# Kernel optimization log

Hardware: AMD Instinct MI355X
Metric: run time of the kernel (lower is better)

## Reference

```python
import jax, jax.numpy as jnp
import numpy as np

B, T, D, H, O = 256, 512, 256, 1024, 256


def _uniform(key, shape, fan_in):
    # kaiming_uniform with a=0.1: bound = sqrt(6 / ((1 + a^2) * fan_in))
    bound = float(np.sqrt(6.0 / ((1.0 + 0.1 ** 2) * fan_in)))
    return jax.random.uniform(key, shape, jnp.float32, -bound, bound)


def setup_inputs() -> dict:
    key = jax.random.key(0)
    ks = jax.random.split(key, 8)
    inp = {
        "x": jax.random.normal(ks[0], (B, T, D), jnp.float32),
        "W_gx": _uniform(ks[1], (D, H), D),
        "W_gh": _uniform(ks[2], (H, H), H),
        "b_g": jnp.zeros((H,), jnp.float32),
        "W_ix": _uniform(ks[3], (D, H), D),
        "W_ih": _uniform(ks[4], (H, H), H),
        "b_i": jnp.zeros((H,), jnp.float32),
        "W_fx": _uniform(ks[5], (D, H), D),
        "W_fh": _uniform(ks[6], (H, H), H),
        "b_f": jnp.zeros((H,), jnp.float32),
        "W_ox": _uniform(jax.random.fold_in(key, 10), (D, H), D),
        "W_oh": _uniform(jax.random.fold_in(key, 11), (H, H), H),
        "b_o": jnp.zeros((H,), jnp.float32),
        "W_ph": _uniform(ks[7], (H, O), H),
        "b_p": jnp.zeros((O,), jnp.float32),
    }
    return inp


def reference(x, W_gx, W_gh, b_g, W_ix, W_ih, b_i, W_fx, W_fh, b_f,
              W_ox, W_oh, b_o, W_ph, b_p):
    Hd = W_gh.shape[0]
    # Fuse the 4 per-gate matmuls into two GEMMs (same math as the loop).
    Wx = jnp.concatenate([W_gx, W_ix, W_fx, W_ox], axis=1)  # [D, 4H]
    Wh = jnp.concatenate([W_gh, W_ih, W_fh, W_oh], axis=1)  # [H, 4H]
    b = jnp.concatenate([b_g, b_i, b_f, b_o])               # [4H]
    xW = jnp.einsum('btd,dk->tbk', x, Wx) + b                # [T, B, 4H]

    def step(carry, xw_t):
        h, c = carry
        z = xw_t + h @ Wh                                    # [B, 4H]
        g = jnp.tanh(z[:, :Hd])
        i = jax.nn.sigmoid(z[:, Hd:2 * Hd])
        f = jax.nn.sigmoid(z[:, 2 * Hd:3 * Hd])
        o = jax.nn.sigmoid(z[:, 3 * Hd:])
        c = g * i + c * f
        h = jnp.tanh(c) * o
        return (h, c), None

    h0 = jnp.zeros((x.shape[0], Hd), x.dtype)
    (h, _), _ = jax.lax.scan(step, (h0, h0), xW)
    return jax.nn.softmax(h @ W_ph + b_p, axis=1)
```

## Files before the change

### kernel.cpp

```cpp
#include <hip/hip_runtime.h>


typedef _Float16 f16;
typedef _Float16 f16x8 __attribute__((ext_vector_type(8)));
typedef _Float16 f16x4 __attribute__((ext_vector_type(4)));
typedef float f32x4 __attribute__((ext_vector_type(4)));
typedef unsigned int u32;

#define WS_WT    0
#define WS_WPHT  10485760
#define WS_HBUF  11010048
#define WS_LG    12058624
#define WS_CNT   12320768
#define WS_TICK  12322816
#define WS_XH    16777216
#define WS_XH_END 83886080

#define ZB    81920u
#define BCAST 114688

__device__ __forceinline__ float sigm(float v) { return 1.0f / (1.0f + __expf(-v)); }
__device__ __forceinline__ float tanhfast(float v) {
  float t = __expf(-2.0f * fabsf(v));
  float r = (1.0f - t) / (1.0f + t);
  return v < 0.0f ? -r : r;
}

__global__ __launch_bounds__(256) void prep_wt(
    const float* __restrict__ Wgh, const float* __restrict__ Wih,
    const float* __restrict__ Wfh, const float* __restrict__ Woh,
    const float* __restrict__ Wgx, const float* __restrict__ Wix,
    const float* __restrict__ Wfx, const float* __restrict__ Wox,
    f16* __restrict__ WT)
{
  __shared__ float tile[32][33];
  int bid = blockIdx.x;
  int gate = bid / 1280;
  int rem  = bid % 1280;
  int jt = rem / 40, kt = rem % 40;
  const float* srcH = (gate==0)?Wgh:(gate==1)?Wih:(gate==2)?Wfh:Woh;
  const float* srcX = (gate==0)?Wgx:(gate==1)?Wix:(gate==2)?Wfx:Wox;
  const float* src = (kt < 32) ? (srcH + (size_t)(kt*32)*1024)
                               : (srcX + (size_t)(kt*32 - 1024)*1024);
  int t = threadIdx.x;
  {
    int jl = t & 31, kg = t >> 5;
#pragma unroll
    for (int it = 0; it < 4; ++it) {
      int kl = kg + it*8;
      tile[kl][jl] = src[(size_t)kl*1024 + jt*32 + jl];
    }
  }
  __syncthreads();
  {
    int kl = t & 31, jg = t >> 5;
#pragma unroll
    for (int it = 0; it < 4; ++it) {
      int jl2 = jg + it*8;
      WT[(size_t)(gate*1024 + jt*32 + jl2)*1280 + kt*32 + kl] = (f16)tile[kl][jl2];
    }
  }
}

__global__ __launch_bounds__(256) void prep_wph(const float* __restrict__ Wph,
                                                f16* __restrict__ WphT)
{
  __shared__ float tile[32][33];
  int bid = blockIdx.x;
  int jt = bid & 7, kt = bid >> 3;
  int t = threadIdx.x;
  {
    int jl = t & 31, kg = t >> 5;
#pragma unroll
    for (int it = 0; it < 4; ++it) {
      int kl = kg + it*8;
      tile[kl][jl] = Wph[(size_t)(kt*32 + kl)*256 + jt*32 + jl];
    }
  }
  __syncthreads();
  {
    int kl = t & 31, jg = t >> 5;
#pragma unroll
    for (int it = 0; it < 4; ++it) {
      int jl2 = jg + it*8;
      WphT[(size_t)(jt*32 + jl2)*1024 + kt*32 + kl] = (f16)tile[kl][jl2];
    }
  }
}

__global__ __launch_bounds__(256) void prep_x16(const float* __restrict__ x,
                                                f16* __restrict__ xh)
{
  size_t i = ((size_t)blockIdx.x*256 + threadIdx.x) * 16;
  const float4* src = (const float4*)(x + i);
  f16x4* dst = (f16x4*)(xh + i);
#pragma unroll
  for (int j = 0; j < 4; ++j) {
    float4 v = src[j];
    f16x4 h; h[0]=(f16)v.x; h[1]=(f16)v.y; h[2]=(f16)v.z; h[3]=(f16)v.w;
    dst[j] = h;
  }
}

__global__ __launch_bounds__(512, 2) void lstm_main(
    const float* __restrict__ x, const f16* __restrict__ xh, int use_xh,
    const f16* __restrict__ WT, const f16* __restrict__ WphT,
    f16* __restrict__ hbuf,
    const float* __restrict__ bgp, const float* __restrict__ bip,
    const float* __restrict__ bfp, const float* __restrict__ bop,
    const float* __restrict__ bpp, float* __restrict__ lg,
    u32* __restrict__ cnt, u32* __restrict__ tick, float* __restrict__ out)
{
  __shared__ __align__(16) char smem[114704];
  const int tid  = threadIdx.x;
  const int lane = tid & 63;
  const int wv   = tid >> 6;
  const int hgrp = wv & 1;
  const int kh   = wv >> 1;
  const int l15 = lane & 15, l4 = lane >> 4;

  u32 myxcd;
  asm volatile("s_getreg_b32 %0, hwreg(HW_REG_XCC_ID)" : "=s"(myxcd));
  myxcd &= 7u;
  if (tid == 0) {
    u32 t = __hip_atomic_fetch_add(tick + myxcd, 1u,
                                   __ATOMIC_RELAXED, __HIP_MEMORY_SCOPE_AGENT);
    *(volatile u32*)(smem + BCAST) = t;
  }
  if (wv == 0) {
    u32 v = 0;
    int guard = 0;
    for (;;) {
      v = (lane < 8) ? __hip_atomic_load(tick + lane, __ATOMIC_RELAXED,
                                         __HIP_MEMORY_SCOPE_AGENT) : 0u;
      u32 sum = v;
      sum += __shfl_xor(sum, 1);
      sum += __shfl_xor(sum, 2);
      sum += __shfl_xor(sum, 4);
      if (__shfl(sum, 0) == 256u) break;
      __builtin_amdgcn_s_sleep(1);
      if (++guard > (1 << 20)) break;
    }
    int even = __all((lane < 8) ? (v == 32u) : 1);
    if (lane == 0) *(volatile u32*)(smem + BCAST + 4) = (u32)even;
  }
  __syncthreads();
  const bool xloc = (*(volatile u32*)(smem + BCAST + 4)) != 0u;
  const u32 myticket = *(volatile u32*)(smem + BCAST);
  const int xg = xloc ? (int)myxcd    : (blockIdx.x & 7);
  const int cg = xloc ? (int)myticket : (blockIdx.x >> 3);
  u32* flg = cnt + xg*64;

  f16x8 Breg[10][4];
  {
    const int gate = l15 & 3, hsub = l15 >> 2;
#pragma unroll
    for (int f = 0; f < 4; ++f) {
      const int n = gate*1024 + cg*32 + hgrp*16 + f*4 + hsub;
      const f16* wb = WT + (size_t)n*1280 + kh*320 + l4*8;
#pragma unroll
      for (int kk = 0; kk < 10; ++kk) {
        Breg[kk][f] = *(const f16x8*)(wb + kk*32);
        asm volatile("" : "+v"(Breg[kk][f]));
      }
    }
  }

  const int bcol = cg*32 + (tid & 31);
  const float bgr = bgp[bcol], bir = bip[bcol], bfr = bfp[bcol], bor = bop[bcol];

  const u32 aoff = (u32)l15*2560u + (u32)(kh*640 + l4*16);
  const u32 aswz = (u32)l15 << 4;
  const int srow = tid >> 5;
  const int sseg = tid & 31;
  const u32 swzr = (u32)srow << 4;

  float cA = 0.0f, cB = 0.0f;

  u32 pre = 0xFFFFFFFFu;
  bool preOK = false;

#pragma unroll 1
  for (int slot = 0; slot < 1024; ++slot) {
    const int T = slot & 1, s = slot >> 1;
    const u32 Abase = (u32)T * 40960u;
    u32* flgT = flg + T*32;
    const int grow = xg*32 + T*16 + srow;

    if (use_xh) {
      const char* xrow = (const char*)xh + ((size_t)grow*512 + (size_t)s)*512;
      uint4 v = *(const uint4*)(xrow + sseg*16);
      *(uint4*)(smem + Abase + (((u32)srow*2560u + 2048u + (u32)sseg*16u) ^ swzr)) = v;
    } else {
      const float* xsrc = x + ((size_t)grow*512 + (size_t)s)*256;
      float4 xv0 = *(const float4*)(xsrc + (sseg     )*4);
      float4 xv1 = *(const float4*)(xsrc + (sseg + 32)*4);
      f16x4 hv;
      hv[0] = (f16)xv0.x; hv[1] = (f16)xv0.y; hv[2] = (f16)xv0.z; hv[3] = (f16)xv0.w;
      *(f16x4*)(smem + Abase + (((u32)srow*2560u + 2048u + 8u*(u32)(sseg     )) ^ swzr)) = hv;
      hv[0] = (f16)xv1.x; hv[1] = (f16)xv1.y; hv[2] = (f16)xv1.z; hv[3] = (f16)xv1.w;
      *(f16x4*)(smem + Abase + (((u32)srow*2560u + 2048u + 8u*(u32)(sseg + 32)) ^ swzr)) = hv;
    }
    if (s > 0 && !preOK) {
      const u32 tgt = (u32)s;
      u32 v = tgt;
      int guard = 0;
      for (;;) {
        if (lane < 32)
          v = __hip_atomic_load(flgT + lane, __ATOMIC_RELAXED,
                                __HIP_MEMORY_SCOPE_AGENT);
        if (__all(v >= tgt)) break;
        __builtin_amdgcn_s_sleep(1);
        if (++guard > (1 << 18)) break;
      }
      if (lane == 0) {
        if (xloc) { asm volatile("buffer_inv sc0\n\ts_waitcnt vmcnt(0)" ::: "memory"); }
        else      { __threadfence(); }
      }
    }
    {
      const f16* hsrc = hbuf + (size_t)(s & 1)*262144 + (size_t)grow*1024;
#pragma unroll
      for (int j = 0; j < 4; ++j) {
        int chunk = sseg + 32*j;
        uint4 v = *(const uint4*)(hsrc + chunk*8);
        *(uint4*)(smem + Abase + (((u32)srow*2560u + 16u*(u32)chunk) ^ swzr)) = v;
      }
    }
    __syncthreads();
    f32x4 acc0 = {}, acc1 = {}, acc2 = {}, acc3 = {};
#pragma unroll
    for (int kk = 0; kk < 10; ++kk) {
      f16x8 av = *(const f16x8*)(smem + Abase + ((aoff + (u32)kk*64u) ^ aswz));
      acc0 = __builtin_amdgcn_mfma_f32_16x16x32_f16(Breg[kk][0], av, acc0, 0, 0, 0);
      acc1 = __builtin_amdgcn_mfma_f32_16x16x32_f16(Breg[kk][1], av, acc1, 0, 0, 0);
      acc2 = __builtin_amdgcn_mfma_f32_16x16x32_f16(Breg[kk][2], av, acc2, 0, 0, 0);
      acc3 = __builtin_amdgcn_mfma_f32_16x16x32_f16(Breg[kk][3], av, acc3, 0, 0, 0);
    }
    {
      const int nT = (slot + 1) & 1, nS = (slot + 1) >> 1;
      pre = 0xFFFFFFFFu;
      if (nS > 0 && nS < 512 && lane < 32)
        pre = __hip_atomic_load(flg + nT*32 + lane, __ATOMIC_RELAXED,
                                __HIP_MEMORY_SCOPE_AGENT);
    }
    {
      const u32 zkh = ZB + (u32)kh*8192u;
#pragma unroll
      for (int f = 0; f < 4; ++f) {
        const u32 hcol = (u32)(hgrp*16 + f*4 + l4);
        const u32 s16 = ((u32)(l15*32) + hcol) ^ ((u32)(l15 & 7));
        f32x4 acc = (f==0)?acc0:(f==1)?acc1:(f==2)?acc2:acc3;
        *(f32x4*)(smem + zkh + s16*16u) = acc;
      }
    }
    __syncthreads();
    {
      f16* hw = hbuf + (size_t)((s & 1) ^ 1)*262144;
      const int row = tid >> 5, hcol = tid & 31;
      const u32 s16 = ((u32)(row*32) + (u32)hcol) ^ ((u32)(row & 7));
      const u32 ro = s16*16u;
      f32x4 z0 = *(const f32x4*)(smem + ZB +        ro);
      f32x4 z1 = *(const f32x4*)(smem + ZB + 8192u  + ro);
      f32x4 z2 = *(const f32x4*)(smem + ZB + 16384u + ro);
      f32x4 z3 = *(const f32x4*)(smem + ZB + 24576u + ro);
      float zg = z0[0] + z1[0] + z2[0] + z3[0] + bgr;
      float zi = z0[1] + z1[1] + z2[1] + z3[1] + bir;
      float zf = z0[2] + z1[2] + z2[2] + z3[2] + bfr;
      float zo = z0[3] + z1[3] + z2[3] + z3[3] + bor;
      float cv = T ? cB : cA;
      float gv = tanhfast(zg);
      float iv = sigm(zi);
      float fv = sigm(zf);
      float ov = sigm(zo);
      float cn = gv*iv + cv*fv;
      if (T) cB = cn; else cA = cn;
      hw[(size_t)(xg*32 + T*16 + row)*1024 + cg*32 + hcol] = (f16)(tanhfast(cn) * ov);
    }
    {
      const int nS = (slot + 1) >> 1;
      bool ok = (nS >= 512) || __all(pre >= (u32)nS);
      preOK = xloc && ok;
      if (preOK && nS < 512 && lane == 0) {
        asm volatile("buffer_inv sc0\n\ts_waitcnt vmcnt(0)" ::: "memory");
      }
    }
    __syncthreads();
    if (tid == 0) {
      if (!xloc) __threadfence();
      __hip_atomic_store(flgT + cg, (u32)(s + 1),
                         __ATOMIC_RELAXED, __HIP_MEMORY_SCOPE_AGENT);
    }
  }

  if (wv == 0) {
    u32 v = 512u;
    int guard = 0;
    for (;;) {
      v = __hip_atomic_load(flg + lane, __ATOMIC_RELAXED,
                            __HIP_MEMORY_SCOPE_AGENT);
      if (__all(v >= 512u)) break;
      __builtin_amdgcn_s_sleep(1);
      if (++guard > (1 << 18)) break;
    }
    if (lane == 0) {
      if (xloc) { asm volatile("buffer_inv sc0\n\ts_waitcnt vmcnt(0)" ::: "memory"); }
      else      { __threadfence(); }
    }
  }
  __syncthreads();
  {
#pragma unroll 1
    for (int p = 0; p < 32; ++p) {
      int rowl = wv*4 + (p >> 3);
      int oc   = p & 7;
      const f16* hp = hbuf + (size_t)(xg*32 + rowl)*1024 + lane*16;
      const f16* wp = WphT + (size_t)(cg*8 + oc)*1024 + lane*16;
      f16x8 h0 = *(const f16x8*)hp;
      f16x8 h1 = *(const f16x8*)(hp + 8);
      f16x8 w0 = *(const f16x8*)wp;
      f16x8 w1 = *(const f16x8*)(wp + 8);
      float sum = 0.f;
#pragma unroll
      for (int q = 0; q < 8; ++q)
        sum += (float)h0[q]*(float)w0[q] + (float)h1[q]*(float)w1[q];
#pragma unroll
      for (int d = 1; d < 64; d <<= 1) sum += __shfl_xor(sum, d);
      if (lane == 0)
        lg[(size_t)(xg*32 + rowl)*256 + cg*8 + oc] = sum + bpp[cg*8 + oc];
    }
  }
  __syncthreads();
  if (tid == 0) {
    if (!xloc) __threadfence();
    __hip_atomic_store(flg + cg, 513u, __ATOMIC_RELAXED, __HIP_MEMORY_SCOPE_AGENT);
  }
  if (wv == 0) {
    u32 v = 513u;
    int guard = 0;
    for (;;) {
      if (lane < 32)
        v = __hip_atomic_load(flg + lane, __ATOMIC_RELAXED, __HIP_MEMORY_SCOPE_AGENT);
      if (__all(v >= 513u)) break;
      __builtin_amdgcn_s_sleep(1);
      if (++guard > (1 << 18)) break;
    }
    if (lane == 0) {
      if (xloc) { asm volatile("buffer_inv sc0\n\ts_waitcnt vmcnt(0)" ::: "memory"); }
      else      { __threadfence(); }
    }
  }
  __syncthreads();
  if (tid < 64) {
    int rowg = xg*32 + cg;
    const float* lr = lg + (size_t)rowg*256;
    float v0 = lr[tid], v1 = lr[tid+64], v2 = lr[tid+128], v3 = lr[tid+192];
    float mx = fmaxf(fmaxf(v0, v1), fmaxf(v2, v3));
#pragma unroll
    for (int d = 1; d < 64; d <<= 1) mx = fmaxf(mx, __shfl_xor(mx, d));
    float e0 = __expf(v0-mx), e1 = __expf(v1-mx), e2 = __expf(v2-mx), e3 = __expf(v3-mx);
    float sm = e0+e1+e2+e3;
#pragma unroll
    for (int d = 1; d < 64; d <<= 1) sm += __shfl_xor(sm, d);
    float inv = 1.0f / sm;
    float* orow = out + (size_t)rowg*256;
    orow[tid]      = e0*inv;
    orow[tid+64]   = e1*inv;
    orow[tid+128]  = e2*inv;
    orow[tid+192]  = e3*inv;
  }
}

extern "C" void kernel_launch(void* const* d_in, const int* in_sizes, int n_in,
                              void* d_out, int out_size, void* d_ws, size_t ws_size,
                              hipStream_t stream) {
  (void)in_sizes; (void)n_in; (void)out_size;
  const float* x   = (const float*)d_in[0];
  const float* Wgx = (const float*)d_in[1];
  const float* Wgh = (const float*)d_in[2];
  const float* bg  = (const float*)d_in[3];
  const float* Wix = (const float*)d_in[4];
  const float* Wih = (const float*)d_in[5];
  const float* bi  = (const float*)d_in[6];
  const float* Wfx = (const float*)d_in[7];
  const float* Wfh = (const float*)d_in[8];
  const float* bf  = (const float*)d_in[9];
  const float* Wox = (const float*)d_in[10];
  const float* Woh = (const float*)d_in[11];
  const float* bo  = (const float*)d_in[12];
  const float* Wph = (const float*)d_in[13];
  const float* bp  = (const float*)d_in[14];

  char* ws = (char*)d_ws;
  f16*   WT   = (f16*)(ws + WS_WT);
  f16*   WphT = (f16*)(ws + WS_WPHT);
  f16*   hbuf = (f16*)(ws + WS_HBUF);
  float* lg   = (float*)(ws + WS_LG);
  u32*   cnt  = (u32*)(ws + WS_CNT);
  u32*   tick = (u32*)(ws + WS_TICK);
  const int use_xh = (ws_size >= (size_t)WS_XH_END) ? 1 : 0;
  f16*   xh   = (f16*)(ws + WS_XH);

  hipMemsetAsync(hbuf, 0, 524288, stream);
  hipMemsetAsync(cnt, 0, 2048 + 64, stream);

  prep_wt<<<5120, 256, 0, stream>>>(Wgh, Wih, Wfh, Woh, Wgx, Wix, Wfx, Wox, WT);
  prep_wph<<<256, 256, 0, stream>>>(Wph, WphT);
  if (use_xh)
    prep_x16<<<8192, 256, 0, stream>>>(x, xh);
  lstm_main<<<256, 512, 0, stream>>>(x, xh, use_xh, WT, WphT, hbuf,
                                     bg, bi, bf, bo, bp,
                                     lg, cnt, tick, (float*)d_out);
}
```

Measured before the change: 2.468 ms.

## Load MFMA A-operands directly from global into registers, drop LDS staging

Each wave now loads its h and x fragments for the MFMA straight from global memory (hbuf and xh/x) into registers, in the layout the MFMA expects. This replaces staging them through a swizzled LDS tile and removes the __syncthreads before the matmul. LDS shrinks to the reduction and broadcast area. The cost is uncoalesced 16-byte global reads per lane, repeated across the waves that share rows, in exchange for fewer LDS round trips and one fewer block-wide barrier per step.

```diff
diff --git a/kernel.cpp b/kernel.cpp
--- a/kernel.cpp
+++ b/kernel.cpp
@@ -16,8 +16,8 @@
 #define WS_XH    16777216
 #define WS_XH_END 83886080
 
-#define ZB    81920u
-#define BCAST 114688
+#define ZB    0u
+#define BCAST 32768
 
 __device__ __forceinline__ float sigm(float v) { return 1.0f / (1.0f + __expf(-v)); }
 __device__ __forceinline__ float tanhfast(float v) {
@@ -111,7 +111,7 @@
     const float* __restrict__ bpp, float* __restrict__ lg,
     u32* __restrict__ cnt, u32* __restrict__ tick, float* __restrict__ out)
 {
-  __shared__ __align__(16) char smem[114704];
+  __shared__ __align__(16) char smem[32784];
   const int tid  = threadIdx.x;
   const int lane = tid & 63;
   const int wv   = tid >> 6;
@@ -169,12 +169,6 @@
   const int bcol = cg*32 + (tid & 31);
   const float bgr = bgp[bcol], bir = bip[bcol], bfr = bfp[bcol], bor = bop[bcol];
 
-  const u32 aoff = (u32)l15*2560u + (u32)(kh*640 + l4*16);
-  const u32 aswz = (u32)l15 << 4;
-  const int srow = tid >> 5;
-  const int sseg = tid & 31;
-  const u32 swzr = (u32)srow << 4;
-
   float cA = 0.0f, cB = 0.0f;
 
   u32 pre = 0xFFFFFFFFu;
@@ -183,23 +177,39 @@
 #pragma unroll 1
   for (int slot = 0; slot < 1024; ++slot) {
     const int T = slot & 1, s = slot >> 1;
-    const u32 Abase = (u32)T * 40960u;
     u32* flgT = flg + T*32;
-    const int grow = xg*32 + T*16 + srow;
-
-    if (use_xh) {
-      const char* xrow = (const char*)xh + ((size_t)grow*512 + (size_t)s)*512;
-      uint4 v = *(const uint4*)(xrow + sseg*16);
-      *(uint4*)(smem + Abase + (((u32)srow*2560u + 2048u + (u32)sseg*16u) ^ swzr)) = v;
-    } else {
-      const float* xsrc = x + ((size_t)grow*512 + (size_t)s)*256;
-      float4 xv0 = *(const float4*)(xsrc + (sseg     )*4);
-      float4 xv1 = *(const float4*)(xsrc + (sseg + 32)*4);
-      f16x4 hv;
-      hv[0] = (f16)xv0.x; hv[1] = (f16)xv0.y; hv[2] = (f16)xv0.z; hv[3] = (f16)xv0.w;
-      *(f16x4*)(smem + Abase + (((u32)srow*2560u + 2048u + 8u*(u32)(sseg     )) ^ swzr)) = hv;
-      hv[0] = (f16)xv1.x; hv[1] = (f16)xv1.y; hv[2] = (f16)xv1.z; hv[3] = (f16)xv1.w;
-      *(f16x4*)(smem + Abase + (((u32)srow*2560u + 2048u + 8u*(u32)(sseg + 32)) ^ swzr)) = hv;
+    const int rowB = xg*32 + T*16 + l15;
+
+    f16x8 bv0, bv1, bv2, bv3, bv4, bv5, bv6, bv7, bv8, bv9;
+    if (kh == 3) {
+      if (use_xh) {
+        const char* xb = (const char*)(xh + (size_t)rowB*131072 + (size_t)s*256)
+                       + l4*16;
+        bv2 = *(const f16x8*)(xb       );
+        bv3 = *(const f16x8*)(xb +  64);
+        bv4 = *(const f16x8*)(xb + 128);
+        bv5 = *(const f16x8*)(xb + 192);
+        bv6 = *(const f16x8*)(xb + 256);
+        bv7 = *(const f16x8*)(xb + 320);
+        bv8 = *(const f16x8*)(xb + 384);
+        bv9 = *(const f16x8*)(xb + 448);
+      } else {
+        const float* xf = x + (size_t)rowB*131072 + (size_t)s*256 + l4*8;
+#pragma unroll
+        for (int kk = 2; kk < 10; ++kk) {
+          float4 a = *(const float4*)(xf + (kk-2)*32);
+          float4 b = *(const float4*)(xf + (kk-2)*32 + 4);
+          f16x8 hv;
+          hv[0]=(f16)a.x; hv[1]=(f16)a.y; hv[2]=(f16)a.z; hv[3]=(f16)a.w;
+          hv[4]=(f16)b.x; hv[5]=(f16)b.y; hv[6]=(f16)b.z; hv[7]=(f16)b.w;
+          switch (kk) {
+            case 2: bv2=hv; break; case 3: bv3=hv; break;
+            case 4: bv4=hv; break; case 5: bv5=hv; break;
+            case 6: bv6=hv; break; case 7: bv7=hv; break;
+            case 8: bv8=hv; break; default: bv9=hv; break;
+          }
+        }
+      }
     }
     if (s > 0 && !preOK) {
       const u32 tgt = (u32)s;
@@ -219,19 +229,29 @@
       }
     }
     {
-      const f16* hsrc = hbuf + (size_t)(s & 1)*262144 + (size_t)grow*1024;
-#pragma unroll
-      for (int j = 0; j < 4; ++j) {
-        int chunk = sseg + 32*j;
-        uint4 v = *(const uint4*)(hsrc + chunk*8);
-        *(uint4*)(smem + Abase + (((u32)srow*2560u + 16u*(u32)chunk) ^ swzr)) = v;
-      }
-    }
-    __syncthreads();
+      const char* hb = (const char*)(hbuf + (size_t)(s & 1)*262144
+                                     + (size_t)rowB*1024) + kh*640 + l4*16;
+      if (kh < 3) {
+        bv0 = *(const f16x8*)(hb       );
+        bv1 = *(const f16x8*)(hb +  64);
+        bv2 = *(const f16x8*)(hb + 128);
+        bv3 = *(const f16x8*)(hb + 192);
+        bv4 = *(const f16x8*)(hb + 256);
+        bv5 = *(const f16x8*)(hb + 320);
+        bv6 = *(const f16x8*)(hb + 384);
+        bv7 = *(const f16x8*)(hb + 448);
+        bv8 = *(const f16x8*)(hb + 512);
+        bv9 = *(const f16x8*)(hb + 576);
+      } else {
+        bv0 = *(const f16x8*)(hb      );
+        bv1 = *(const f16x8*)(hb + 64);
+      }
+    }
     f32x4 acc0 = {}, acc1 = {}, acc2 = {}, acc3 = {};
 #pragma unroll
     for (int kk = 0; kk < 10; ++kk) {
-      f16x8 av = *(const f16x8*)(smem + Abase + ((aoff + (u32)kk*64u) ^ aswz));
+      f16x8 av = (kk==0)?bv0:(kk==1)?bv1:(kk==2)?bv2:(kk==3)?bv3:(kk==4)?bv4:
+                 (kk==5)?bv5:(kk==6)?bv6:(kk==7)?bv7:(kk==8)?bv8:bv9;
       acc0 = __builtin_amdgcn_mfma_f32_16x16x32_f16(Breg[kk][0], av, acc0, 0, 0, 0);
       acc1 = __builtin_amdgcn_mfma_f32_16x16x32_f16(Breg[kk][1], av, acc1, 0, 0, 0);
       acc2 = __builtin_amdgcn_mfma_f32_16x16x32_f16(Breg[kk][2], av, acc2, 0, 0, 0);
```

Result: slower. 3.709 ms (+50.3%).

## Process both 16-row halves per step instead of alternating half-batch slots

Applied to the files above, without the earlier changes.

The recurrent loop used to alternate two 16-row sub-batches across 1024 slots, each with its own flag set, so one half's barrier wait could overlap with the other half's compute. Now each of the 512 steps loads all 32 rows, runs twice the MFMAs on shared B registers, and reduces both halves together with a single flag array. This halves the number of grid-wide flag waits and __syncthreads rounds per sequence step and raises MFMA work per barrier. In exchange it gives up the two-phase overlap between halves and enlarges LDS use to about 144 KB, which may limit occupancy.

```diff
diff --git a/kernel.cpp b/kernel.cpp
--- a/kernel.cpp
+++ b/kernel.cpp
@@ -17,7 +17,7 @@
 #define WS_XH_END 83886080
 
 #define ZB    81920u
-#define BCAST 114688
+#define BCAST 147456
 
 __device__ __forceinline__ float sigm(float v) { return 1.0f / (1.0f + __expf(-v)); }
 __device__ __forceinline__ float tanhfast(float v) {
@@ -111,7 +111,7 @@
     const float* __restrict__ bpp, float* __restrict__ lg,
     u32* __restrict__ cnt, u32* __restrict__ tick, float* __restrict__ out)
 {
-  __shared__ __align__(16) char smem[114704];
+  __shared__ __align__(16) char smem[147472];
   const int tid  = threadIdx.x;
   const int lane = tid & 63;
   const int wv   = tid >> 6;
@@ -169,37 +169,40 @@
   const int bcol = cg*32 + (tid & 31);
   const float bgr = bgp[bcol], bir = bip[bcol], bfr = bfp[bcol], bor = bop[bcol];
 
-  const u32 aoff = (u32)l15*2560u + (u32)(kh*640 + l4*16);
-  const u32 aswz = (u32)l15 << 4;
-  const int srow = tid >> 5;
-  const int sseg = tid & 31;
-  const u32 swzr = (u32)srow << 4;
-
-  float cA = 0.0f, cB = 0.0f;
+  const u32 aoff0 = (u32)l15*2560u + (u32)(kh*640 + l4*16);
+  const u32 aoff1 = aoff0 + 16u*2560u;
+  const u32 aswz  = (u32)l15 << 4;
+  const int srow = tid >> 4;
+  const int sseg = tid & 15;
+  const u32 swzr = ((u32)(srow & 15)) << 4;
+
+  float c0 = 0.0f, c1 = 0.0f;
 
   u32 pre = 0xFFFFFFFFu;
   bool preOK = false;
 
 #pragma unroll 1
-  for (int slot = 0; slot < 1024; ++slot) {
-    const int T = slot & 1, s = slot >> 1;
-    const u32 Abase = (u32)T * 40960u;
-    u32* flgT = flg + T*32;
-    const int grow = xg*32 + T*16 + srow;
+  for (int s = 0; s < 512; ++s) {
+    const int grow = xg*32 + srow;
 
     if (use_xh) {
       const char* xrow = (const char*)xh + ((size_t)grow*512 + (size_t)s)*512;
-      uint4 v = *(const uint4*)(xrow + sseg*16);
-      *(uint4*)(smem + Abase + (((u32)srow*2560u + 2048u + (u32)sseg*16u) ^ swzr)) = v;
+      uint4 v0 = *(const uint4*)(xrow + sseg*16);
+      uint4 v1 = *(const uint4*)(xrow + (sseg + 16)*16);
+      *(uint4*)(smem + (((u32)srow*2560u + 2048u + (u32)sseg*16u) ^ swzr)) = v0;
+      *(uint4*)(smem + (((u32)srow*2560u + 2048u + (u32)(sseg+16)*16u) ^ swzr)) = v1;
     } else {
       const float* xsrc = x + ((size_t)grow*512 + (size_t)s)*256;
-      float4 xv0 = *(const float4*)(xsrc + (sseg     )*4);
-      float4 xv1 = *(const float4*)(xsrc + (sseg + 32)*4);
-      f16x4 hv;
-      hv[0] = (f16)xv0.x; hv[1] = (f16)xv0.y; hv[2] = (f16)xv0.z; hv[3] = (f16)xv0.w;
-      *(f16x4*)(smem + Abase + (((u32)srow*2560u + 2048u + 8u*(u32)(sseg     )) ^ swzr)) = hv;
-      hv[0] = (f16)xv1.x; hv[1] = (f16)xv1.y; hv[2] = (f16)xv1.z; hv[3] = (f16)xv1.w;
-      *(f16x4*)(smem + Abase + (((u32)srow*2560u + 2048u + 8u*(u32)(sseg + 32)) ^ swzr)) = hv;
+#pragma unroll
+      for (int j = 0; j < 2; ++j) {
+        int cc = sseg + 16*j;
+        float4 a = *(const float4*)(xsrc + cc*8);
+        float4 b = *(const float4*)(xsrc + cc*8 + 4);
+        f16x8 hv;
+        hv[0]=(f16)a.x; hv[1]=(f16)a.y; hv[2]=(f16)a.z; hv[3]=(f16)a.w;
+        hv[4]=(f16)b.x; hv[5]=(f16)b.y; hv[6]=(f16)b.z; hv[7]=(f16)b.w;
+        *(f16x8*)(smem + (((u32)srow*2560u + 2048u + (u32)cc*16u) ^ swzr)) = hv;
+      }
     }
     if (s > 0 && !preOK) {
       const u32 tgt = (u32)s;
@@ -207,7 +210,7 @@
       int guard = 0;
       for (;;) {
         if (lane < 32)
-          v = __hip_atomic_load(flgT + lane, __ATOMIC_RELAXED,
+          v = __hip_atomic_load(flg + lane, __ATOMIC_RELAXED,
                                 __HIP_MEMORY_SCOPE_AGENT);
         if (__all(v >= tgt)) break;
         __builtin_amdgcn_s_sleep(1);
@@ -221,64 +224,78 @@
     {
       const f16* hsrc = hbuf + (size_t)(s & 1)*262144 + (size_t)grow*1024;
 #pragma unroll
-      for (int j = 0; j < 4; ++j) {
-        int chunk = sseg + 32*j;
+      for (int j = 0; j < 8; ++j) {
+        int chunk = sseg + 16*j;
         uint4 v = *(const uint4*)(hsrc + chunk*8);
-        *(uint4*)(smem + Abase + (((u32)srow*2560u + 16u*(u32)chunk) ^ swzr)) = v;
+        *(uint4*)(smem + (((u32)srow*2560u + 16u*(u32)chunk) ^ swzr)) = v;
       }
     }
     __syncthreads();
-    f32x4 acc0 = {}, acc1 = {}, acc2 = {}, acc3 = {};
+    f32x4 a00 = {}, a01 = {}, a02 = {}, a03 = {};
+    f32x4 a10 = {}, a11 = {}, a12 = {}, a13 = {};
 #pragma unroll
     for (int kk = 0; kk < 10; ++kk) {
-      f16x8 av = *(const f16x8*)(smem + Abase + ((aoff + (u32)kk*64u) ^ aswz));
-      acc0 = __builtin_amdgcn_mfma_f32_16x16x32_f16(Breg[kk][0], av, acc0, 0, 0, 0);
-      acc1 = __builtin_amdgcn_mfma_f32_16x16x32_f16(Breg[kk][1], av, acc1, 0, 0, 0);
-      acc2 = __builtin_amdgcn_mfma_f32_16x16x32_f16(Breg[kk][2], av, acc2, 0, 0, 0);
-      acc3 = __builtin_amdgcn_mfma_f32_16x16x32_f16(Breg[kk][3], av, acc3, 0, 0, 0);
+      f16x8 av0 = *(const f16x8*)(smem + ((aoff0 + (u32)kk*64u) ^ aswz));
+      f16x8 av1 = *(const f16x8*)(smem + ((aoff1 + (u32)kk*64u) ^ aswz));
+      a00 = __builtin_amdgcn_mfma_f32_16x16x32_f16(Breg[kk][0], av0, a00, 0, 0, 0);
+      a01 = __builtin_amdgcn_mfma_f32_16x16x32_f16(Breg[kk][1], av0, a01, 0, 0, 0);
+      a02 = __builtin_amdgcn_mfma_f32_16x16x32_f16(Breg[kk][2], av0, a02, 0, 0, 0);
+      a03 = __builtin_amdgcn_mfma_f32_16x16x32_f16(Breg[kk][3], av0, a03, 0, 0, 0);
+      a10 = __builtin_amdgcn_mfma_f32_16x16x32_f16(Breg[kk][0], av1, a10, 0, 0, 0);
+      a11 = __builtin_amdgcn_mfma_f32_16x16x32_f16(Breg[kk][1], av1, a11, 0, 0, 0);
+      a12 = __builtin_amdgcn_mfma_f32_16x16x32_f16(Breg[kk][2], av1, a12, 0, 0, 0);
+      a13 = __builtin_amdgcn_mfma_f32_16x16x32_f16(Breg[kk][3], av1, a13, 0, 0, 0);
     }
     {
-      const int nT = (slot + 1) & 1, nS = (slot + 1) >> 1;
+      const int nS = s + 1;
       pre = 0xFFFFFFFFu;
-      if (nS > 0 && nS < 512 && lane < 32)
-        pre = __hip_atomic_load(flg + nT*32 + lane, __ATOMIC_RELAXED,
+      if (nS < 512 && lane < 32)
+        pre = __hip_atomic_load(flg + lane, __ATOMIC_RELAXED,
                                 __HIP_MEMORY_SCOPE_AGENT);
     }
     {
-      const u32 zkh = ZB + (u32)kh*8192u;
+      const u32 zkh = ZB + (u32)kh*16384u;
 #pragma unroll
       for (int f = 0; f < 4; ++f) {
         const u32 hcol = (u32)(hgrp*16 + f*4 + l4);
-        const u32 s16 = ((u32)(l15*32) + hcol) ^ ((u32)(l15 & 7));
-        f32x4 acc = (f==0)?acc0:(f==1)?acc1:(f==2)?acc2:acc3;
-        *(f32x4*)(smem + zkh + s16*16u) = acc;
+        const u32 r0 = (u32)l15, r1 = (u32)(l15 + 16);
+        const u32 s0 = ((r0*32u) + hcol) ^ (r0 & 7u);
+        const u32 s1 = ((r1*32u) + hcol) ^ (r1 & 7u);
+        f32x4 p0 = (f==0)?a00:(f==1)?a01:(f==2)?a02:a03;
+        f32x4 p1 = (f==0)?a10:(f==1)?a11:(f==2)?a12:a13;
+        *(f32x4*)(smem + zkh + s0*16u) = p0;
+        *(f32x4*)(smem + zkh + s1*16u) = p1;
       }
     }
     __syncthreads();
     {
       f16* hw = hbuf + (size_t)((s & 1) ^ 1)*262144;
-      const int row = tid >> 5, hcol = tid & 31;
-      const u32 s16 = ((u32)(row*32) + (u32)hcol) ^ ((u32)(row & 7));
-      const u32 ro = s16*16u;
-      f32x4 z0 = *(const f32x4*)(smem + ZB +        ro);
-      f32x4 z1 = *(const f32x4*)(smem + ZB + 8192u  + ro);
-      f32x4 z2 = *(const f32x4*)(smem + ZB + 16384u + ro);
-      f32x4 z3 = *(const f32x4*)(smem + ZB + 24576u + ro);
-      float zg = z0[0] + z1[0] + z2[0] + z3[0] + bgr;
-      float zi = z0[1] + z1[1] + z2[1] + z3[1] + bir;
-      float zf = z0[2] + z1[2] + z2[2] + z3[2] + bfr;
-      float zo = z0[3] + z1[3] + z2[3] + z3[3] + bor;
-      float cv = T ? cB : cA;
-      float gv = tanhfast(zg);
-      float iv = sigm(zi);
-      float fv = sigm(zf);
-      float ov = sigm(zo);
-      float cn = gv*iv + cv*fv;
-      if (T) cB = cn; else cA = cn;
-      hw[(size_t)(xg*32 + T*16 + row)*1024 + cg*32 + hcol] = (f16)(tanhfast(cn) * ov);
+      const int hcol = tid & 31;
+#pragma unroll
+      for (int e2 = 0; e2 < 2; ++e2) {
+        const int row = (tid >> 5) + e2*16;
+        const u32 s16 = ((u32)(row*32) + (u32)hcol) ^ ((u32)(row & 7));
+        const u32 ro = s16*16u;
+        f32x4 z0 = *(const f32x4*)(smem + ZB +          ro);
+        f32x4 z1 = *(const f32x4*)(smem + ZB + 16384u + ro);
+        f32x4 z2 = *(const f32x4*)(smem + ZB + 32768u + ro);
+        f32x4 z3 = *(const f32x4*)(smem + ZB + 49152u + ro);
+        float zg = z0[0] + z1[0] + z2[0] + z3[0] + bgr;
+        float zi = z0[1] + z1[1] + z2[1] + z3[1] + bir;
+        float zf = z0[2] + z1[2] + z2[2] + z3[2] + bfr;
+        float zo = z0[3] + z1[3] + z2[3] + z3[3] + bor;
+        float cv = e2 ? c1 : c0;
+        float gv = tanhfast(zg);
+        float iv = sigm(zi);
+        float fv = sigm(zf);
+        float ov = sigm(zo);
+        float cn = gv*iv + cv*fv;
+        if (e2) c1 = cn; else c0 = cn;
+        hw[(size_t)(xg*32 + row)*1024 + cg*32 + hcol] = (f16)(tanhfast(cn) * ov);
+      }
     }
     {
-      const int nS = (slot + 1) >> 1;
+      const int nS = s + 1;
       bool ok = (nS >= 512) || __all(pre >= (u32)nS);
       preOK = xloc && ok;
       if (preOK && nS < 512 && lane == 0) {
@@ -288,7 +305,7 @@
     __syncthreads();
     if (tid == 0) {
       if (!xloc) __threadfence();
-      __hip_atomic_store(flgT + cg, (u32)(s + 1),
+      __hip_atomic_store(flg + cg, (u32)(s + 1),
                          __ATOMIC_RELAXED, __HIP_MEMORY_SCOPE_AGENT);
     }
   }
@@ -297,8 +314,9 @@
     u32 v = 512u;
     int guard = 0;
     for (;;) {
-      v = __hip_atomic_load(flg + lane, __ATOMIC_RELAXED,
-                            __HIP_MEMORY_SCOPE_AGENT);
+      if (lane < 32)
+        v = __hip_atomic_load(flg + lane, __ATOMIC_RELAXED,
+                              __HIP_MEMORY_SCOPE_AGENT);
       if (__all(v >= 512u)) break;
       __builtin_amdgcn_s_sleep(1);
       if (++guard > (1 << 18)) break;
```

Result: slower. 2.795 ms (+13.3%).
